# Kernel tuning notes

Hardware: AMD Instinct MI355X
Metric: run time of the kernel (lower is better)

Reference implementation:

```python
import jax, jax.numpy as jnp
import numpy as np

EPS = 1e-05  # epsilon from __init__
K, D = 2048, 256  # codebook_size, embed dim (hardcoded in module)
B, T = 8, 8192


def setup_inputs() -> dict:
    key = jax.random.key(0)
    k1, k2, k3 = jax.random.split(key, 3)
    hidden_states = jax.random.normal(k1, (B, T, D), dtype=jnp.float32)
    embed_sum = jax.random.normal(k2, (K, D), dtype=jnp.float32)
    # cluster_usage starts as ones in the module; use positive random counts
    cluster_usage = jax.random.uniform(k3, (K,), dtype=jnp.float32) * 10.0 + 0.5
    return {"hidden_states": hidden_states, "embed_sum": embed_sum, "cluster_usage": cluster_usage}


def reference(hidden_states, embed_sum, cluster_usage):
    # embed property: embed_sum / clamp(cluster_usage, min=eps)[:, None]
    embed = embed_sum / jnp.clip(cluster_usage, EPS, None)[:, None]  # [K, D]

    shape = hidden_states.shape
    x = hidden_states.reshape(-1, shape[-1]).astype(jnp.float32)  # [N, D]

    x2 = jnp.sum(x * x, axis=-1, keepdims=True)        # [N, 1]
    e2 = jnp.sum(embed * embed, axis=-1)               # [K]
    d2 = x2 - 2.0 * (x @ embed.T) + e2[None, :]        # [N, K] -- the big intermediate

    embed_ind = jnp.argmin(d2, axis=-1).reshape(shape[:-1])  # [B, T]
    # decode: embedding lookup of selected codes
    quantized = jnp.take(embed, embed_ind, axis=0)            # [B, T, D]
    return embed_ind, quantized
```

## Files before the change

### kernel.cpp

```cpp
#include <hip/hip_runtime.h>
#include <hip/hip_bf16.h>


typedef float f32x4 __attribute__((ext_vector_type(4)));
typedef short s16x8 __attribute__((ext_vector_type(8)));
typedef _Float16 h16x8 __attribute__((ext_vector_type(8)));

#define D_DIM 256
#define N_ROWS 65536
#define K_CODES 2048
#define VQ_EPS 1e-5f
#define DELTA 0.25f

__device__ __forceinline__ short f16s(float f) {
    _Float16 h = (_Float16)f;
    return __builtin_bit_cast(short, h);
}
__device__ __forceinline__ unsigned fkey(float f) {
    unsigned u = __float_as_uint(f);
    return u ^ (unsigned)(((int)u >> 31) | (int)0x80000000);
}
__device__ __forceinline__ float funkey(unsigned k) {
    unsigned u = (k & 0x80000000u) ? (k ^ 0x80000000u) : ~k;
    return __uint_as_float(u);
}
__device__ __forceinline__ unsigned med3u(unsigned a, unsigned b, unsigned c) {
    unsigned d;
    asm("v_med3_u32 %0, %1, %2, %3" : "=v"(d) : "v"(a), "v"(b), "v"(c));
    return d;
}
__device__ __forceinline__ void gload16(const void* g, void* l) {
    __builtin_amdgcn_global_load_lds(
        (const __attribute__((address_space(1))) void*)g,
        (__attribute__((address_space(3))) void*)l, 16, 0, 0);
}

#define DPP_ROR(v, N) \
    ((unsigned)__builtin_amdgcn_update_dpp((int)(v), (int)(v), 0x120 + (N), 0xF, 0xF, true))

__device__ __forceinline__ void np_sumsq_16lane(const float* a, float* out, int g) {
#pragma clang fp contract(off)
    int j = g & 7, h = g >> 3;
    const float* p = a + h * 128;
    float t = p[j];
    float r = t * t;
#pragma unroll
    for (int i = 1; i < 16; ++i) { float v = p[j + 8 * i]; r += v * v; }
    r += __shfl_xor(r, 1);
    r += __shfl_xor(r, 2);
    r += __shfl_xor(r, 4);
    float other = __shfl_xor(r, 8);
    if (g == 0) *out = r + other;
}

__global__ void prep_all(const float* __restrict__ es, const float* __restrict__ us,
                         const float* __restrict__ x,
                         float* __restrict__ embed, unsigned short* __restrict__ eswz,
                         float* __restrict__ e2,
                         unsigned short* __restrict__ xswz, float* __restrict__ x2) {
    __shared__ float le[8][256];
    const int tid = threadIdx.x;
    if (blockIdx.x < 256) {
        const int rloc = tid >> 5, idx = tid & 31;
        const int r = blockIdx.x * 8 + rloc;
        const float u = fmaxf(us[r], VQ_EPS);
        f32x4 v0 = *(const f32x4*)&es[r * D_DIM + idx * 8];
        f32x4 v1 = *(const f32x4*)&es[r * D_DIM + idx * 8 + 4];
        f32x4 e0, e1;
#pragma unroll
        for (int j = 0; j < 4; ++j) { e0[j] = v0[j] / u; e1[j] = v1[j] / u; }
        *(f32x4*)&embed[r * D_DIM + idx * 8] = e0;
        *(f32x4*)&embed[r * D_DIM + idx * 8 + 4] = e1;
        *(f32x4*)&le[rloc][idx * 8] = e0;
        *(f32x4*)&le[rloc][idx * 8 + 4] = e1;
        int kc = idx >> 2, ss = idx & 3;
        int sd = ss ^ ((r >> 1) & 3);
        s16x8 b;
#pragma unroll
        for (int j = 0; j < 4; ++j) { b[j] = f16s(e0[j]); b[j + 4] = f16s(e1[j]); }
        *(s16x8*)&eswz[r * 256 + kc * 32 + sd * 8] = b;
        __syncthreads();
        if (idx < 16) np_sumsq_16lane(&le[rloc][0], &e2[r], idx);
    } else {
        int gid = (blockIdx.x - 256) * 256 + tid;
        int r = gid >> 5, idx = gid & 31;
        int kc = idx >> 2, s = idx & 3;
        int k0 = kc * 32 + (s ^ ((r >> 1) & 3)) * 8;
        const float* p = x + r * D_DIM + k0;
        s16x8 v;
#pragma unroll
        for (int j = 0; j < 8; ++j) v[j] = f16s(p[j]);
        *(s16x8*)&xswz[r * 256 + kc * 32 + s * 8] = v;
        if (idx < 16)
            np_sumsq_16lane(x + r * D_DIM, x2 + r, idx);
    }
}

__launch_bounds__(256, 2)
__global__ void vq_scan(const unsigned short* __restrict__ xswz,
                        const unsigned short* __restrict__ eswz,
                        const float* __restrict__ e2,
                        uint4* __restrict__ keys) {
    __shared__ __align__(16) short lds[2][2][4096];

    const int bid = blockIdx.x;
    const int swz = (bid & 7) * 1024 + (bid >> 3);
    const int mt = swz >> 4, nt = swz & 15;
    const int m_base = mt * 128, n_base = nt * 128;
    const int tid = threadIdx.x, lane = tid & 63, wid = tid >> 6;
    const int rb = wid * 32;
    const int l15 = lane & 15, lg = lane >> 4;

    f32x4 acc[2][8];
#pragma unroll
    for (int m = 0; m < 2; ++m)
#pragma unroll
        for (int n = 0; n < 8; ++n) { f32x4 z = {0.f, 0.f, 0.f, 0.f}; acc[m][n] = z; }

    auto stage = [&](int buf, int kc) {
#pragma unroll
        for (int i = 0; i < 2; ++i) {
            int off = i * 4096 + wid * 1024 + lane * 16;
            int row = off >> 6, slot = (off >> 4) & 3;
            gload16((const char*)xswz + (((size_t)(m_base + row)) << 9) + (kc << 6) + (slot << 4),
                    (char*)&lds[buf][0][0] + off);
            gload16((const char*)eswz + (((size_t)(n_base + row)) << 9) + (kc << 6) + (slot << 4),
                    (char*)&lds[buf][1][0] + off);
        }
    };
    auto compute = [&](int buf) {
        const short* A = &lds[buf][0][0];
        const short* B = &lds[buf][1][0];
        h16x8 af[2], bf[8];
#pragma unroll
        for (int m = 0; m < 2; ++m) {
            int R = rb + m * 16 + l15, s = lg ^ ((R >> 1) & 3);
            af[m] = __builtin_bit_cast(h16x8, *(const s16x8*)&A[R * 32 + s * 8]);
        }
#pragma unroll
        for (int n = 0; n < 8; ++n) {
            int R = n * 16 + l15, s = lg ^ ((R >> 1) & 3);
            bf[n] = __builtin_bit_cast(h16x8, *(const s16x8*)&B[R * 32 + s * 8]);
        }
#pragma unroll
        for (int m = 0; m < 2; ++m)
#pragma unroll
            for (int n = 0; n < 8; ++n)
                acc[m][n] = __builtin_amdgcn_mfma_f32_16x16x32_f16(af[m], bf[n], acc[m][n], 0, 0, 0);
    };

    stage(0, 0);
    __syncthreads();
#pragma unroll 1
    for (int kc = 0; kc < 8; ++kc) {
        if (kc < 7) stage((kc + 1) & 1, kc + 1);
        compute(kc & 1);
        __syncthreads();
    }

    const int grow0 = m_base + rb + lg * 4;
    float e2v[8];
#pragma unroll
    for (int n = 0; n < 8; ++n) e2v[n] = e2[n_base + n * 16 + l15];

#pragma unroll
    for (int m = 0; m < 2; ++m) {
#pragma unroll
        for (int j = 0; j < 4; ++j) {
            int gr = grow0 + m * 16 + j;
            unsigned k1 = 0xFFFFFFFFu, k2 = 0xFFFFFFFFu;
            unsigned k3 = 0xFFFFFFFFu, k4 = 0xFFFFFFFFu;
#pragma unroll
            for (int n = 0; n < 8; ++n) {
                float sv = __builtin_fmaf(-2.0f, acc[m][n][j], e2v[n]);
                unsigned pk = (fkey(sv) & 0xFFFFF800u)
                              | (unsigned)(n_base + n * 16 + l15);
                unsigned n1 = min(pk, k1);
                unsigned n2 = med3u(pk, k1, k2);
                unsigned n3 = med3u(pk, k2, k3);
                unsigned n4 = med3u(pk, k3, k4);
                k1 = n1; k2 = n2; k3 = n3; k4 = n4;
            }
#define MERGE_STEP(RR)                                                         \
            {                                                                  \
                unsigned o1 = DPP_ROR(k1, RR), o2 = DPP_ROR(k2, RR);           \
                unsigned o3 = DPP_ROR(k3, RR), o4 = DPP_ROR(k4, RR);           \
                unsigned c1 = min(k1, o4), c2 = min(k2, o3);                   \
                unsigned c3 = min(k3, o2), c4 = min(k4, o1);                   \
                unsigned t;                                                    \
                t = min(c1, c3); c3 = max(c1, c3); c1 = t;                     \
                t = min(c2, c4); c4 = max(c2, c4); c2 = t;                     \
                t = min(c1, c2); c2 = max(c1, c2); c1 = t;                     \
                t = min(c3, c4); c4 = max(c3, c4); c3 = t;                     \
                k1 = c1; k2 = c2; k3 = c3; k4 = c4;                            \
            }
            MERGE_STEP(8)
            MERGE_STEP(4)
            MERGE_STEP(2)
            MERGE_STEP(1)
#undef MERGE_STEP
            if (l15 == 0) {
                uint4 kq; kq.x = k1; kq.y = k2; kq.z = k3; kq.w = k4;
                keys[gr * 16 + nt] = kq;
            }
        }
    }
}

__launch_bounds__(256, 4)
__global__ void vq_rescore(const float* __restrict__ x, const float* __restrict__ embed,
                           const float* __restrict__ e2, const float* __restrict__ x2,
                           const uint4* __restrict__ keys,
                           const float* __restrict__ es, const float* __restrict__ us,
                           float* __restrict__ out) {
    __shared__ float lx[4][256];
    __shared__ float le[4][8][260];
    __shared__ int lcode[4][64];

    const int tid = threadIdx.x, w = tid >> 6, lane = tid & 63;
    const int r = blockIdx.x * 4 + w;
    const int t16 = lane & 15;
    const float x2v = x2[r];
    const unsigned long long lt = (1ull << lane) - 1ull;

    *(f32x4*)&lx[w][lane * 4] = *(const f32x4*)&x[r * D_DIM + lane * 4];

    uint4 kq = keys[r * 16 + t16];
    unsigned kmin = kq.x & 0xFFFFF800u;
#pragma unroll
    for (int s = 1; s < 16; s <<= 1) {
        unsigned ok = __shfl_xor(kmin, s);
        kmin = ok < kmin ? ok : kmin;
    }
    const float thr = funkey(kmin) + DELTA;

    unsigned sv[4] = {kq.x, kq.y, kq.z, kq.w};
    int nc = 0;
#pragma unroll
    for (int s = 0; s < 4; ++s) {
        bool v = (lane < 16) && (funkey(sv[s] & 0xFFFFF800u) <= thr);
        unsigned long long b = __ballot(v);
        if (v) lcode[w][nc + __popcll(b & lt)] = (int)(sv[s] & 0x7FFu);
        nc += (int)__popcll(b);
    }
    bool resc = (lane < 16) && (funkey(kq.w & 0xFFFFF800u) <= thr);
    unsigned long long rmask = __ballot(resc);

    float bv = __builtin_inff();
    int bi = 0x7FFFFFFF;
    auto lexmin = [&](float d2, int code) {
        if (d2 < bv || (d2 == bv && code < bi)) { bv = d2; bi = code; }
    };

#pragma unroll 1
    for (int g = 0; g < (nc + 7) >> 3; ++g) {
#pragma unroll
        for (int v = 0; v < 8; ++v) {
            int idx = g * 8 + v;
            if (idx < nc) {
                int code = lcode[w][idx];
                *(f32x4*)&le[w][v][lane * 4] =
                    *(const f32x4*)&embed[code * D_DIM + lane * 4];
            }
        }
        int idx = g * 8 + lane;
        if (lane < 8 && idx < nc) {
            int code = lcode[w][idx];
            float t = 0.0f;
#pragma unroll 8
            for (int k4 = 0; k4 < 64; ++k4) {
                f32x4 a4 = *(const f32x4*)&lx[w][k4 * 4];
                f32x4 e4 = *(const f32x4*)&le[w][lane][k4 * 4];
                t = __builtin_fmaf(a4[0], e4[0], t);
                t = __builtin_fmaf(a4[1], e4[1], t);
                t = __builtin_fmaf(a4[2], e4[2], t);
                t = __builtin_fmaf(a4[3], e4[3], t);
            }
            lexmin((x2v - 2.0f * t) + e2[code], code);
        }
    }

    while (rmask) {
        int t2 = __ffsll(rmask) - 1;
        rmask &= rmask - 1;
        int ca = t2 * 128 + lane, cb = ca + 64;
        float ta = 0.0f, tb = 0.0f;
#pragma unroll 8
        for (int k4 = 0; k4 < 64; ++k4) {
            f32x4 a4 = *(const f32x4*)&lx[w][k4 * 4];
            f32x4 ea = *(const f32x4*)&embed[ca * D_DIM + k4 * 4];
            f32x4 eb = *(const f32x4*)&embed[cb * D_DIM + k4 * 4];
            ta = __builtin_fmaf(a4[0], ea[0], ta);
            tb = __builtin_fmaf(a4[0], eb[0], tb);
            ta = __builtin_fmaf(a4[1], ea[1], ta);
            tb = __builtin_fmaf(a4[1], eb[1], tb);
            ta = __builtin_fmaf(a4[2], ea[2], ta);
            tb = __builtin_fmaf(a4[2], eb[2], tb);
            ta = __builtin_fmaf(a4[3], ea[3], ta);
            tb = __builtin_fmaf(a4[3], eb[3], tb);
        }
        lexmin((x2v - 2.0f * ta) + e2[ca], ca);
        lexmin((x2v - 2.0f * tb) + e2[cb], cb);
    }

#pragma unroll
    for (int s = 1; s < 64; s <<= 1) {
        float ov = __shfl_xor(bv, s);
        int oi = __shfl_xor(bi, s);
        if (ov < bv || (ov == bv && oi < bi)) { bv = ov; bi = oi; }
    }
    if (lane == 0) out[r] = (float)bi;

    float u = fmaxf(us[bi], VQ_EPS);
    f32x4 wv = *(const f32x4*)&es[bi * D_DIM + lane * 4];
    f32x4 o;
#pragma unroll
    for (int j = 0; j < 4; ++j) o[j] = wv[j] / u;
    *(f32x4*)&out[N_ROWS + r * D_DIM + lane * 4] = o;
}

extern "C" void kernel_launch(void* const* d_in, const int* in_sizes, int n_in,
                              void* d_out, int out_size, void* d_ws, size_t ws_size,
                              hipStream_t stream) {
    const float* x = (const float*)d_in[0];
    const float* es = (const float*)d_in[1];
    const float* us = (const float*)d_in[2];
    float* out = (float*)d_out;

    char* w = (char*)d_ws;
    unsigned short* xswz = (unsigned short*)(w);
    unsigned short* eswz = (unsigned short*)(w + 33554432);
    float* embed         = (float*)(w + 34603008);
    float* e2            = (float*)(w + 36700160);
    float* x2            = (float*)(w + 36708352);
    uint4* keys          = (uint4*)(w + 36970496);

    hipLaunchKernelGGL(prep_all, dim3(8448), dim3(256), 0, stream,
                       es, us, x, embed, eswz, e2, xswz, x2);
    hipLaunchKernelGGL(vq_scan, dim3(8192), dim3(256), 0, stream,
                       xswz, eswz, e2, keys);
    hipLaunchKernelGGL(vq_rescore, dim3(16384), dim3(256), 0, stream,
                       x, embed, e2, x2, keys, es, us, out);
}
```

Measured before the change: 207.1 us.

## Shrink per-tile candidate list to top-3 with biased positive-float keys

The scan epilogue now keeps a top-3 instead of a top-4 candidate list per row per 128-code tile. It adds a constant bias to the scores so they stay positive and can be compared as raw float bits without the sign-flip key transform. The key packs only a 7-bit local code index, which keeps more mantissa bits, and rescore rebuilds the global code from the tile position. This cuts min/med3/DPP work in the epilogue and shrinks key storage from 16 to 12 bytes per tile. The risk is that a true nearest code ranked fourth within a tile is no longer considered, and that scores could go negative if they exceed the bias.

```diff
diff --git a/kernel.cpp b/kernel.cpp
--- a/kernel.cpp
+++ b/kernel.cpp
@@ -11,18 +11,12 @@
 #define K_CODES 2048
 #define VQ_EPS 1e-5f
 #define DELTA 0.25f
+#define KBIAS 4096.0f
+#define KMASK 0xFFFFFF80u
 
 __device__ __forceinline__ short f16s(float f) {
     _Float16 h = (_Float16)f;
     return __builtin_bit_cast(short, h);
-}
-__device__ __forceinline__ unsigned fkey(float f) {
-    unsigned u = __float_as_uint(f);
-    return u ^ (unsigned)(((int)u >> 31) | (int)0x80000000);
-}
-__device__ __forceinline__ float funkey(unsigned k) {
-    unsigned u = (k & 0x80000000u) ? (k ^ 0x80000000u) : ~k;
-    return __uint_as_float(u);
 }
 __device__ __forceinline__ unsigned med3u(unsigned a, unsigned b, unsigned c) {
     unsigned d;
@@ -100,7 +94,7 @@
 __global__ void vq_scan(const unsigned short* __restrict__ xswz,
                         const unsigned short* __restrict__ eswz,
                         const float* __restrict__ e2,
-                        uint4* __restrict__ keys) {
+                        uint2* __restrict__ keys2, unsigned* __restrict__ keys3) {
     __shared__ __align__(16) short lds[2][2][4096];
 
     const int bid = blockIdx.x;
@@ -159,40 +153,36 @@
     }
 
     const int grow0 = m_base + rb + lg * 4;
-    float e2v[8];
-#pragma unroll
-    for (int n = 0; n < 8; ++n) e2v[n] = e2[n_base + n * 16 + l15];
+    float e2b[8];
+#pragma unroll
+    for (int n = 0; n < 8; ++n) e2b[n] = e2[n_base + n * 16 + l15] + KBIAS;
 
 #pragma unroll
     for (int m = 0; m < 2; ++m) {
 #pragma unroll
         for (int j = 0; j < 4; ++j) {
             int gr = grow0 + m * 16 + j;
-            unsigned k1 = 0xFFFFFFFFu, k2 = 0xFFFFFFFFu;
-            unsigned k3 = 0xFFFFFFFFu, k4 = 0xFFFFFFFFu;
+            unsigned k1 = 0xFFFFFFFFu, k2 = 0xFFFFFFFFu, k3 = 0xFFFFFFFFu;
 #pragma unroll
             for (int n = 0; n < 8; ++n) {
-                float sv = __builtin_fmaf(-2.0f, acc[m][n][j], e2v[n]);
-                unsigned pk = (fkey(sv) & 0xFFFFF800u)
-                              | (unsigned)(n_base + n * 16 + l15);
+                float sv = __builtin_fmaf(-2.0f, acc[m][n][j], e2b[n]);
+                unsigned pk = (__float_as_uint(sv) & KMASK)
+                              | (unsigned)(n * 16 + l15);
                 unsigned n1 = min(pk, k1);
                 unsigned n2 = med3u(pk, k1, k2);
                 unsigned n3 = med3u(pk, k2, k3);
-                unsigned n4 = med3u(pk, k3, k4);
-                k1 = n1; k2 = n2; k3 = n3; k4 = n4;
+                k1 = n1; k2 = n2; k3 = n3;
             }
 #define MERGE_STEP(RR)                                                         \
             {                                                                  \
                 unsigned o1 = DPP_ROR(k1, RR), o2 = DPP_ROR(k2, RR);           \
-                unsigned o3 = DPP_ROR(k3, RR), o4 = DPP_ROR(k4, RR);           \
-                unsigned c1 = min(k1, o4), c2 = min(k2, o3);                   \
-                unsigned c3 = min(k3, o2), c4 = min(k4, o1);                   \
+                unsigned o3 = DPP_ROR(k3, RR);                                 \
+                unsigned c1 = min(k1, o3), c2 = min(k2, o2), c3 = min(k3, o1); \
                 unsigned t;                                                    \
-                t = min(c1, c3); c3 = max(c1, c3); c1 = t;                     \
-                t = min(c2, c4); c4 = max(c2, c4); c2 = t;                     \
                 t = min(c1, c2); c2 = max(c1, c2); c1 = t;                     \
-                t = min(c3, c4); c4 = max(c3, c4); c3 = t;                     \
-                k1 = c1; k2 = c2; k3 = c3; k4 = c4;                            \
+                t = min(c2, c3); c3 = max(c2, c3); c2 = t;                     \
+                t = min(c1, c2); c2 = max(c1, c2); c1 = t;                     \
+                k1 = c1; k2 = c2; k3 = c3;                                     \
             }
             MERGE_STEP(8)
             MERGE_STEP(4)
@@ -200,8 +190,9 @@
             MERGE_STEP(1)
 #undef MERGE_STEP
             if (l15 == 0) {
-                uint4 kq; kq.x = k1; kq.y = k2; kq.z = k3; kq.w = k4;
-                keys[gr * 16 + nt] = kq;
+                uint2 kq; kq.x = k1; kq.y = k2;
+                keys2[gr * 16 + nt] = kq;
+                keys3[gr * 16 + nt] = k3;
             }
         }
     }
@@ -210,7 +201,8 @@
 __launch_bounds__(256, 4)
 __global__ void vq_rescore(const float* __restrict__ x, const float* __restrict__ embed,
                            const float* __restrict__ e2, const float* __restrict__ x2,
-                           const uint4* __restrict__ keys,
+                           const uint2* __restrict__ keys2,
+                           const unsigned* __restrict__ keys3,
                            const float* __restrict__ es, const float* __restrict__ us,
                            float* __restrict__ out) {
     __shared__ float lx[4][256];
@@ -225,25 +217,27 @@
 
     *(f32x4*)&lx[w][lane * 4] = *(const f32x4*)&x[r * D_DIM + lane * 4];
 
-    uint4 kq = keys[r * 16 + t16];
-    unsigned kmin = kq.x & 0xFFFFF800u;
+    uint2 k12 = keys2[r * 16 + t16];
+    unsigned k3v = keys3[r * 16 + t16];
+    unsigned kmin = k12.x & KMASK;
 #pragma unroll
     for (int s = 1; s < 16; s <<= 1) {
         unsigned ok = __shfl_xor(kmin, s);
         kmin = ok < kmin ? ok : kmin;
     }
-    const float thr = funkey(kmin) + DELTA;
-
-    unsigned sv[4] = {kq.x, kq.y, kq.z, kq.w};
+    const float thr = __uint_as_float(kmin) + DELTA;
+
+    unsigned sv[3] = {k12.x, k12.y, k3v};
     int nc = 0;
 #pragma unroll
-    for (int s = 0; s < 4; ++s) {
-        bool v = (lane < 16) && (funkey(sv[s] & 0xFFFFF800u) <= thr);
+    for (int s = 0; s < 3; ++s) {
+        bool v = (lane < 16) && (__uint_as_float(sv[s] & KMASK) <= thr);
         unsigned long long b = __ballot(v);
-        if (v) lcode[w][nc + __popcll(b & lt)] = (int)(sv[s] & 0x7FFu);
+        if (v) lcode[w][nc + __popcll(b & lt)] =
+                   (int)(sv[s] & 0x7Fu) + t16 * 128;
         nc += (int)__popcll(b);
     }
-    bool resc = (lane < 16) && (funkey(kq.w & 0xFFFFF800u) <= thr);
+    bool resc = (lane < 16) && (__uint_as_float(k3v & KMASK) <= thr);
     unsigned long long rmask = __ballot(resc);
 
     float bv = __builtin_inff();
@@ -333,12 +327,13 @@
     float* embed         = (float*)(w + 34603008);
     float* e2            = (float*)(w + 36700160);
     float* x2            = (float*)(w + 36708352);
-    uint4* keys          = (uint4*)(w + 36970496);
+    uint2* keys2         = (uint2*)(w + 36970496);
+    unsigned* keys3      = (unsigned*)(w + 45359104);
 
     hipLaunchKernelGGL(prep_all, dim3(8448), dim3(256), 0, stream,
                        es, us, x, embed, eswz, e2, xswz, x2);
     hipLaunchKernelGGL(vq_scan, dim3(8192), dim3(256), 0, stream,
-                       xswz, eswz, e2, keys);
+                       xswz, eswz, e2, keys2, keys3);
     hipLaunchKernelGGL(vq_rescore, dim3(16384), dim3(256), 0, stream,
-                       x, embed, e2, x2, keys, es, us, out);
-}
+                       x, embed, e2, x2, keys2, keys3, es, us, out);
+}
```

After: 204.7 us. Within noise of the previous version (-1.2%).
